# Performance work log

Measured on AMD Instinct MI355X. Metric: run time of the kernel, lower is better.

The kernel has to match this reference:

```python
import jax, jax.numpy as jnp
import numpy as np

EMBED_SIZE = 128
SCALE = EMBED_SIZE ** (-0.5)


def setup_inputs() -> dict:
    key = jax.random.key(0)
    kq, kk, kv = jax.random.split(key, 3)
    B, S, E = 16, 2048, EMBED_SIZE
    return {
        "query": jax.random.normal(kq, (B, S, E), dtype=jnp.float32),
        "key": jax.random.normal(kk, (B, S, E), dtype=jnp.float32),
        "value": jax.random.normal(kv, (B, S, E), dtype=jnp.float32),
    }


def reference(query, key, value):
    # scores: [B, S, S] = q @ k^T, scaled by embed_size**-0.5
    scores = jnp.einsum("bqe,bke->bqk", query, key) * SCALE
    probs = jax.nn.softmax(scores, axis=-1)
    # dropout_p = 0.0 -> identity (deterministic reference)
    out = jnp.einsum("bqk,bke->bqe", probs, value)
    return out
```

## Files before the change

### kernel.cpp

```cpp
#include <hip/hip_runtime.h>

#define SEQ 2048
#define EMB 128
#define KT 64
#define QT 64
#define NT 256
#define NITER (SEQ / KT)

typedef __attribute__((ext_vector_type(8))) short short8;
typedef __attribute__((ext_vector_type(4))) float floatx4;
typedef __attribute__((ext_vector_type(4))) unsigned short ushort4_t;

__device__ __forceinline__ unsigned short f2bf(float x) {
  union { float f; unsigned u; } c; c.f = x;
  return (unsigned short)((c.u + 0x7fffu + ((c.u >> 16) & 1u)) >> 16);
}
__device__ __forceinline__ unsigned packbf(float a, float b) {
  return (unsigned)f2bf(a) | ((unsigned)f2bf(b) << 16);
}

__global__ void prep_kernel(const float* __restrict__ K, unsigned short* __restrict__ Kb,
                            const float* __restrict__ V, unsigned short* __restrict__ Vtb,
                            int nblkK) {
  const int tid = threadIdx.x;
  if ((int)blockIdx.x < nblkK) {
    int i = blockIdx.x * NT + tid;
    float4 v = ((const float4*)K)[i];
    ((ushort4_t*)Kb)[i] = (ushort4_t){f2bf(v.x), f2bf(v.y), f2bf(v.z), f2bf(v.w)};
    return;
  }
  const int rb = blockIdx.x - nblkK;
  const int s0 = (rb & 31) * 64;
  const int e0 = ((rb >> 5) & 1) * 64;
  const int b  = rb >> 6;
  const float* src = V + (size_t)b * SEQ * EMB;
  unsigned short* dst = Vtb + (size_t)b * EMB * SEQ;
  const int k = (tid & 15) * 4;
  const int e = (tid >> 4) * 4;
  const float* vb = src + (size_t)(s0 + k) * EMB + e0 + e;
  float4 r0 = *(const float4*)(vb);
  float4 r1 = *(const float4*)(vb + EMB);
  float4 r2 = *(const float4*)(vb + 2 * EMB);
  float4 r3 = *(const float4*)(vb + 3 * EMB);
  unsigned short* d0 = dst + (size_t)(e0 + e) * SEQ + s0 + k;
  *(ushort4_t*)(d0)           = (ushort4_t){f2bf(r0.x), f2bf(r1.x), f2bf(r2.x), f2bf(r3.x)};
  *(ushort4_t*)(d0 + SEQ)     = (ushort4_t){f2bf(r0.y), f2bf(r1.y), f2bf(r2.y), f2bf(r3.y)};
  *(ushort4_t*)(d0 + 2 * SEQ) = (ushort4_t){f2bf(r0.z), f2bf(r1.z), f2bf(r2.z), f2bf(r3.z)};
  *(ushort4_t*)(d0 + 3 * SEQ) = (ushort4_t){f2bf(r0.w), f2bf(r1.w), f2bf(r2.w), f2bf(r3.w)};
}

__global__ __launch_bounds__(NT, 2)
void fattn4(const float* __restrict__ Qp, const unsigned short* __restrict__ Kb,
            const unsigned short* __restrict__ Vtb, float* __restrict__ Op) {
  __shared__ __align__(16) unsigned short Ks[2][KT][EMB];
  __shared__ __align__(16) unsigned short Vs[2][EMB][KT];

  const int tid  = threadIdx.x;
  const int lane = tid & 63;
  const int w    = tid >> 6;
  const int n16  = lane & 15, quad = lane >> 4;
  const int b    = blockIdx.y, q0 = blockIdx.x * QT;
  const size_t bo = (size_t)b * SEQ * EMB;

  auto* ks3 = (__attribute__((address_space(3))) unsigned short*)&Ks[0][0][0];
  auto* vs3 = (__attribute__((address_space(3))) unsigned short*)&Vs[0][0][0];
  const unsigned short* ksl = &Ks[0][0][0];
  const unsigned short* vsl = &Vs[0][0][0];

  const int krw = tid >> 4, kgs = tid & 15;
  const int vrw = tid >> 3, vgs = tid & 7;
  const unsigned short* pK = Kb + bo + (size_t)krw * EMB + (size_t)((kgs ^ (krw & 7)) * 8);
  const unsigned short* pV = Vtb + bo + (size_t)vrw * SEQ + (size_t)((vgs ^ (vrw & 7)) * 8);

  short8 qf[4];
  {
    const float* qr = Qp + bo + (size_t)(q0 + w * 16 + n16) * EMB + quad * 8;
#pragma unroll
    for (int e = 0; e < 4; ++e) {
      float4 x = *(const float4*)(qr + e * 32);
      float4 y = *(const float4*)(qr + e * 32 + 4);
      qf[e] = (short8){(short)f2bf(x.x), (short)f2bf(x.y), (short)f2bf(x.z), (short)f2bf(x.w),
                       (short)f2bf(y.x), (short)f2bf(y.y), (short)f2bf(y.z), (short)f2bf(y.w)};
    }
  }

  int koff[4], voff[2];
#pragma unroll
  for (int e = 0; e < 4; ++e) koff[e] = ((e * 4 + quad) ^ (n16 & 7)) * 8;
#pragma unroll
  for (int k = 0; k < 2; ++k) voff[k] = ((k * 4 + quad) ^ (n16 & 7)) * 8;

  floatx4 o[8];
#pragma unroll
  for (int t = 0; t < 8; ++t) o[t] = (floatx4){0.f, 0.f, 0.f, 0.f};
  float l_part = 0.f;

  const float SCALE = 0.08838834764831845f;
  const float L2E = 1.4426950408889634f;
  const float C1 = SCALE * L2E;

  auto issue = [&](int buf) {
    auto* kb = ks3 + buf * (KT * EMB) + w * 512;
    auto* vb = vs3 + buf * (EMB * KT) + w * 512;
    const unsigned short* gv = pV;
#pragma unroll
    for (int j = 0; j < 4; ++j) {
      __builtin_amdgcn_global_load_lds((const __attribute__((address_space(1))) void*)pK,
                                       (__attribute__((address_space(3))) void*)(kb + j * 2048), 16, 0, 0);
      pK += 2048;
      __builtin_amdgcn_global_load_lds((const __attribute__((address_space(1))) void*)gv,
                                       (__attribute__((address_space(3))) void*)(vb + j * 2048), 16, 0, 0);
      gv += 32 * SEQ;
    }
    pV += KT;
  };

  issue(0);

  const int L1 = n16 + ((quad & 1) ? 32 : 0);
  const int L2v = L1 + 16;
  const bool hi = quad >= 2;

  for (int it = 0; it < NITER; ++it) {
    const int cur = it & 1;
    __syncthreads();
    if (it + 1 < NITER) issue(cur ^ 1);

    floatx4 s[4];
#pragma unroll
    for (int f = 0; f < 4; ++f) s[f] = (floatx4){0.f, 0.f, 0.f, 0.f};
    const unsigned short* kbase = ksl + cur * (KT * EMB);
#pragma unroll
    for (int e = 0; e < 4; ++e) {
#pragma unroll
      for (int f = 0; f < 4; ++f) {
        short8 ak = *(const short8*)(kbase + (f * 16 + n16) * EMB + koff[e]);
        s[f] = __builtin_amdgcn_mfma_f32_16x16x32_bf16(ak, qf[e], s[f], 0, 0, 0);
      }
    }

    float p[4][4];
#pragma unroll
    for (int f = 0; f < 4; ++f)
#pragma unroll
      for (int i = 0; i < 4; ++i) {
        p[f][i] = __builtin_amdgcn_exp2f(s[f][i] * C1);
        l_part += p[f][i];
      }
    unsigned pf0[4], pf1[4];
#pragma unroll
    for (int f = 0; f < 4; ++f) { pf0[f] = packbf(p[f][0], p[f][1]); pf1[f] = packbf(p[f][2], p[f][3]); }

    const unsigned short* vbase = vsl + cur * (EMB * KT);
#pragma unroll
    for (int k0 = 0; k0 < 2; ++k0) {
      const int f0 = k0 * 2, f1 = f0 + 1;
      unsigned a0 = __shfl(pf0[f0], L1), a1 = __shfl(pf1[f0], L1);
      unsigned a2 = __shfl(pf0[f0], L2v), a3 = __shfl(pf1[f0], L2v);
      unsigned b0 = __shfl(pf0[f1], L1), b1 = __shfl(pf1[f1], L1);
      unsigned b2 = __shfl(pf0[f1], L2v), b3 = __shfl(pf1[f1], L2v);
      union { unsigned u[4]; short8 v; } bf;
      bf.u[0] = hi ? b0 : a0;
      bf.u[1] = hi ? b1 : a1;
      bf.u[2] = hi ? b2 : a2;
      bf.u[3] = hi ? b3 : a3;
#pragma unroll
      for (int t = 0; t < 8; ++t) {
        short8 av = *(const short8*)(vbase + (t * 16 + n16) * KT + voff[k0]);
        o[t] = __builtin_amdgcn_mfma_f32_16x16x32_bf16(av, bf.v, o[t], 0, 0, 0);
      }
    }
  }

  float l = l_part;
  l += __shfl_xor(l, 16);
  l += __shfl_xor(l, 32);
  const float inv = 1.0f / l;
  float* orow = Op + bo + (size_t)(q0 + w * 16 + n16) * EMB + quad * 4;
#pragma unroll
  for (int t = 0; t < 8; ++t) {
    float4 st = {o[t][0] * inv, o[t][1] * inv, o[t][2] * inv, o[t][3] * inv};
    *(float4*)(orow + t * 16) = st;
  }
}

extern "C" void kernel_launch(void* const* d_in, const int* in_sizes, int n_in,
                              void* d_out, int out_size, void* d_ws, size_t ws_size,
                              hipStream_t stream) {
  const float* Q = (const float*)d_in[0];
  const float* K = (const float*)d_in[1];
  const float* V = (const float*)d_in[2];
  float* O = (float*)d_out;
  const int B = in_sizes[0] / (SEQ * EMB);
  const size_t tsz = (size_t)B * SEQ * EMB;

  unsigned short* Kb = (unsigned short*)d_ws;
  unsigned short* Vtb = Kb + tsz;

  const int nblkK = (int)(tsz / 4 / NT);
  const int nblkV = (SEQ / 64) * (EMB / 64) * B;
  prep_kernel<<<nblkK + nblkV, NT, 0, stream>>>(K, Kb, V, Vtb, nblkK);
  fattn4<<<dim3(SEQ / QT, B), NT, 0, stream>>>(Q, Kb, Vtb, O);
}
```

Baseline: 157.0 us.

## Split key range across warps and load K/V fragments directly from global

Reorganizes the attention kernel so that each warp covers 32 queries and half of every 64-key tile (a 2x2 warp grid over queries and keys). K and V fragments now load straight from global memory into registers, with no LDS staging, no double buffering and no per-iteration block barrier. The two key-halves are combined at the end through a shared-memory reduction of the output and the row sums. This removes LDS traffic and synchronization, but global-load latency is no longer hidden by a prefetch pipeline, and each K/V tile is fetched by two warps instead of once per block.

```diff
diff --git a/kernel.cpp b/kernel.cpp
--- a/kernel.cpp
+++ b/kernel.cpp
@@ -50,137 +50,147 @@
 }
 
 __global__ __launch_bounds__(NT, 2)
-void fattn4(const float* __restrict__ Qp, const unsigned short* __restrict__ Kb,
+void fattn5(const float* __restrict__ Qp, const unsigned short* __restrict__ Kb,
             const unsigned short* __restrict__ Vtb, float* __restrict__ Op) {
-  __shared__ __align__(16) unsigned short Ks[2][KT][EMB];
-  __shared__ __align__(16) unsigned short Vs[2][EMB][KT];
+  __shared__ __align__(16) float Ored[2][32][132];
+  __shared__ float lred[2][32];
 
   const int tid  = threadIdx.x;
   const int lane = tid & 63;
   const int w    = tid >> 6;
   const int n16  = lane & 15, quad = lane >> 4;
+  const int wq   = w & 1;
+  const int wk   = w >> 1;
   const int b    = blockIdx.y, q0 = blockIdx.x * QT;
   const size_t bo = (size_t)b * SEQ * EMB;
 
-  auto* ks3 = (__attribute__((address_space(3))) unsigned short*)&Ks[0][0][0];
-  auto* vs3 = (__attribute__((address_space(3))) unsigned short*)&Vs[0][0][0];
-  const unsigned short* ksl = &Ks[0][0][0];
-  const unsigned short* vsl = &Vs[0][0][0];
-
-  const int krw = tid >> 4, kgs = tid & 15;
-  const int vrw = tid >> 3, vgs = tid & 7;
-  const unsigned short* pK = Kb + bo + (size_t)krw * EMB + (size_t)((kgs ^ (krw & 7)) * 8);
-  const unsigned short* pV = Vtb + bo + (size_t)vrw * SEQ + (size_t)((vgs ^ (vrw & 7)) * 8);
-
-  short8 qf[4];
-  {
-    const float* qr = Qp + bo + (size_t)(q0 + w * 16 + n16) * EMB + quad * 8;
+  short8 qf[2][4];
+#pragma unroll
+  for (int nt = 0; nt < 2; ++nt) {
+    const float* qr = Qp + bo + (size_t)(q0 + wq * 32 + nt * 16 + n16) * EMB + quad * 8;
 #pragma unroll
     for (int e = 0; e < 4; ++e) {
       float4 x = *(const float4*)(qr + e * 32);
       float4 y = *(const float4*)(qr + e * 32 + 4);
-      qf[e] = (short8){(short)f2bf(x.x), (short)f2bf(x.y), (short)f2bf(x.z), (short)f2bf(x.w),
-                       (short)f2bf(y.x), (short)f2bf(y.y), (short)f2bf(y.z), (short)f2bf(y.w)};
+      qf[nt][e] = (short8){(short)f2bf(x.x), (short)f2bf(x.y), (short)f2bf(x.z), (short)f2bf(x.w),
+                           (short)f2bf(y.x), (short)f2bf(y.y), (short)f2bf(y.z), (short)f2bf(y.w)};
     }
   }
 
-  int koff[4], voff[2];
-#pragma unroll
-  for (int e = 0; e < 4; ++e) koff[e] = ((e * 4 + quad) ^ (n16 & 7)) * 8;
-#pragma unroll
-  for (int k = 0; k < 2; ++k) voff[k] = ((k * 4 + quad) ^ (n16 & 7)) * 8;
-
-  floatx4 o[8];
-#pragma unroll
-  for (int t = 0; t < 8; ++t) o[t] = (floatx4){0.f, 0.f, 0.f, 0.f};
-  float l_part = 0.f;
+  const unsigned short* pK = Kb + bo + (size_t)(wk * 32 + n16) * EMB + quad * 8;
+  const unsigned short* pV = Vtb + bo + (size_t)n16 * SEQ + wk * 32 + quad * 8;
+
+  floatx4 o[8][2];
+#pragma unroll
+  for (int t = 0; t < 8; ++t)
+#pragma unroll
+    for (int nt = 0; nt < 2; ++nt) o[t][nt] = (floatx4){0.f, 0.f, 0.f, 0.f};
+  float lp[2] = {0.f, 0.f};
 
   const float SCALE = 0.08838834764831845f;
   const float L2E = 1.4426950408889634f;
   const float C1 = SCALE * L2E;
 
-  auto issue = [&](int buf) {
-    auto* kb = ks3 + buf * (KT * EMB) + w * 512;
-    auto* vb = vs3 + buf * (EMB * KT) + w * 512;
-    const unsigned short* gv = pV;
-#pragma unroll
-    for (int j = 0; j < 4; ++j) {
-      __builtin_amdgcn_global_load_lds((const __attribute__((address_space(1))) void*)pK,
-                                       (__attribute__((address_space(3))) void*)(kb + j * 2048), 16, 0, 0);
-      pK += 2048;
-      __builtin_amdgcn_global_load_lds((const __attribute__((address_space(1))) void*)gv,
-                                       (__attribute__((address_space(3))) void*)(vb + j * 2048), 16, 0, 0);
-      gv += 32 * SEQ;
-    }
-    pV += KT;
-  };
-
-  issue(0);
-
   const int L1 = n16 + ((quad & 1) ? 32 : 0);
   const int L2v = L1 + 16;
   const bool hi = quad >= 2;
 
   for (int it = 0; it < NITER; ++it) {
-    const int cur = it & 1;
-    __syncthreads();
-    if (it + 1 < NITER) issue(cur ^ 1);
-
-    floatx4 s[4];
-#pragma unroll
-    for (int f = 0; f < 4; ++f) s[f] = (floatx4){0.f, 0.f, 0.f, 0.f};
-    const unsigned short* kbase = ksl + cur * (KT * EMB);
-#pragma unroll
-    for (int e = 0; e < 4; ++e) {
-#pragma unroll
-      for (int f = 0; f < 4; ++f) {
-        short8 ak = *(const short8*)(kbase + (f * 16 + n16) * EMB + koff[e]);
-        s[f] = __builtin_amdgcn_mfma_f32_16x16x32_bf16(ak, qf[e], s[f], 0, 0, 0);
+    short8 kf[2][4];
+#pragma unroll
+    for (int mt = 0; mt < 2; ++mt)
+#pragma unroll
+      for (int e = 0; e < 4; ++e)
+        kf[mt][e] = *(const short8*)(pK + (size_t)mt * 16 * EMB + e * 32);
+    short8 vf[8];
+#pragma unroll
+    for (int t = 0; t < 8; ++t)
+      vf[t] = *(const short8*)(pV + (size_t)t * 16 * SEQ);
+    pK += (size_t)KT * EMB;
+    pV += KT;
+
+    floatx4 s[2][2];
+#pragma unroll
+    for (int mt = 0; mt < 2; ++mt)
+#pragma unroll
+      for (int nt = 0; nt < 2; ++nt) s[mt][nt] = (floatx4){0.f, 0.f, 0.f, 0.f};
+#pragma unroll
+    for (int e = 0; e < 4; ++e)
+#pragma unroll
+      for (int mt = 0; mt < 2; ++mt)
+#pragma unroll
+        for (int nt = 0; nt < 2; ++nt)
+          s[mt][nt] = __builtin_amdgcn_mfma_f32_16x16x32_bf16(kf[mt][e], qf[nt][e], s[mt][nt], 0, 0, 0);
+
+    unsigned pf[2][2][2];
+#pragma unroll
+    for (int mt = 0; mt < 2; ++mt)
+#pragma unroll
+      for (int nt = 0; nt < 2; ++nt) {
+        float p0 = __builtin_amdgcn_exp2f(s[mt][nt][0] * C1);
+        float p1 = __builtin_amdgcn_exp2f(s[mt][nt][1] * C1);
+        float p2 = __builtin_amdgcn_exp2f(s[mt][nt][2] * C1);
+        float p3 = __builtin_amdgcn_exp2f(s[mt][nt][3] * C1);
+        lp[nt] += (p0 + p1) + (p2 + p3);
+        pf[mt][nt][0] = packbf(p0, p1);
+        pf[mt][nt][1] = packbf(p2, p3);
       }
-    }
-
-    float p[4][4];
-#pragma unroll
-    for (int f = 0; f < 4; ++f)
-#pragma unroll
-      for (int i = 0; i < 4; ++i) {
-        p[f][i] = __builtin_amdgcn_exp2f(s[f][i] * C1);
-        l_part += p[f][i];
-      }
-    unsigned pf0[4], pf1[4];
-#pragma unroll
-    for (int f = 0; f < 4; ++f) { pf0[f] = packbf(p[f][0], p[f][1]); pf1[f] = packbf(p[f][2], p[f][3]); }
-
-    const unsigned short* vbase = vsl + cur * (EMB * KT);
-#pragma unroll
-    for (int k0 = 0; k0 < 2; ++k0) {
-      const int f0 = k0 * 2, f1 = f0 + 1;
-      unsigned a0 = __shfl(pf0[f0], L1), a1 = __shfl(pf1[f0], L1);
-      unsigned a2 = __shfl(pf0[f0], L2v), a3 = __shfl(pf1[f0], L2v);
-      unsigned b0 = __shfl(pf0[f1], L1), b1 = __shfl(pf1[f1], L1);
-      unsigned b2 = __shfl(pf0[f1], L2v), b3 = __shfl(pf1[f1], L2v);
+
+    short8 bfr[2];
+#pragma unroll
+    for (int nt = 0; nt < 2; ++nt) {
+      unsigned a0 = __shfl(pf[0][nt][0], L1),  b0 = __shfl(pf[1][nt][0], L1);
+      unsigned a1 = __shfl(pf[0][nt][1], L1),  b1 = __shfl(pf[1][nt][1], L1);
+      unsigned a2 = __shfl(pf[0][nt][0], L2v), b2 = __shfl(pf[1][nt][0], L2v);
+      unsigned a3 = __shfl(pf[0][nt][1], L2v), b3 = __shfl(pf[1][nt][1], L2v);
       union { unsigned u[4]; short8 v; } bf;
       bf.u[0] = hi ? b0 : a0;
       bf.u[1] = hi ? b1 : a1;
       bf.u[2] = hi ? b2 : a2;
       bf.u[3] = hi ? b3 : a3;
-#pragma unroll
-      for (int t = 0; t < 8; ++t) {
-        short8 av = *(const short8*)(vbase + (t * 16 + n16) * KT + voff[k0]);
-        o[t] = __builtin_amdgcn_mfma_f32_16x16x32_bf16(av, bf.v, o[t], 0, 0, 0);
+      bfr[nt] = bf.v;
+    }
+
+#pragma unroll
+    for (int t = 0; t < 8; ++t)
+#pragma unroll
+      for (int nt = 0; nt < 2; ++nt)
+        o[t][nt] = __builtin_amdgcn_mfma_f32_16x16x32_bf16(vf[t], bfr[nt], o[t][nt], 0, 0, 0);
+  }
+
+#pragma unroll
+  for (int nt = 0; nt < 2; ++nt) {
+    lp[nt] += __shfl_xor(lp[nt], 16);
+    lp[nt] += __shfl_xor(lp[nt], 32);
+  }
+
+  if (wk) {
+#pragma unroll
+    for (int t = 0; t < 8; ++t)
+#pragma unroll
+      for (int nt = 0; nt < 2; ++nt)
+        *(floatx4*)&Ored[wq][nt * 16 + n16][t * 16 + quad * 4] = o[t][nt];
+    if (quad == 0) {
+      lred[wq][n16] = lp[0];
+      lred[wq][16 + n16] = lp[1];
+    }
+  }
+  __syncthreads();
+  if (!wk) {
+    float inv[2];
+#pragma unroll
+    for (int nt = 0; nt < 2; ++nt)
+      inv[nt] = 1.0f / (lp[nt] + lred[wq][nt * 16 + n16]);
+#pragma unroll
+    for (int t = 0; t < 8; ++t)
+#pragma unroll
+      for (int nt = 0; nt < 2; ++nt) {
+        floatx4 r = *(const floatx4*)&Ored[wq][nt * 16 + n16][t * 16 + quad * 4];
+        const int q = q0 + wq * 32 + nt * 16 + n16;
+        float4 st = {(o[t][nt][0] + r[0]) * inv[nt], (o[t][nt][1] + r[1]) * inv[nt],
+                     (o[t][nt][2] + r[2]) * inv[nt], (o[t][nt][3] + r[3]) * inv[nt]};
+        *(float4*)(Op + bo + (size_t)q * EMB + t * 16 + quad * 4) = st;
       }
-    }
-  }
-
-  float l = l_part;
-  l += __shfl_xor(l, 16);
-  l += __shfl_xor(l, 32);
-  const float inv = 1.0f / l;
-  float* orow = Op + bo + (size_t)(q0 + w * 16 + n16) * EMB + quad * 4;
-#pragma unroll
-  for (int t = 0; t < 8; ++t) {
-    float4 st = {o[t][0] * inv, o[t][1] * inv, o[t][2] * inv, o[t][3] * inv};
-    *(float4*)(orow + t * 16) = st;
   }
 }
 
@@ -200,5 +210,5 @@
   const int nblkK = (int)(tsz / 4 / NT);
   const int nblkV = (SEQ / 64) * (EMB / 64) * B;
   prep_kernel<<<nblkK + nblkV, NT, 0, stream>>>(K, Kb, V, Vtb, nblkK);
-  fattn4<<<dim3(SEQ / QT, B), NT, 0, stream>>>(Q, Kb, Vtb, O);
-}
+  fattn5<<<dim3(SEQ / QT, B), NT, 0, stream>>>(Q, Kb, Vtb, O);
+}
```

Result: slower. 210.7 us (+34.2%).
